# Performance work log

Hardware: AMD Instinct MI355X
Metric: run time of the kernel (lower is better)

Reference implementation:

```python
import jax, jax.numpy as jnp
import numpy as np

COST_CLASS, COST_BBOX, COST_GIOU = 2.0, 5.0, 2.0
ALPHA, GAMMA = 0.25, 2.0
EPS = 1e-8
N_CANDIDATE = 10


def box_cxcywh_to_xyxy(b):
    cx, cy, w, h = b[..., 0], b[..., 1], b[..., 2], b[..., 3]
    return jnp.stack([cx - 0.5 * w, cy - 0.5 * h, cx + 0.5 * w, cy + 0.5 * h], axis=-1)


def pairwise_iou_giou(b1, b2):
    # b1: [N,4] xyxy, b2: [M,4] xyxy -> iou [N,M], giou [N,M]
    area1 = (b1[:, 2] - b1[:, 0]) * (b1[:, 3] - b1[:, 1])
    area2 = (b2[:, 2] - b2[:, 0]) * (b2[:, 3] - b2[:, 1])
    lt = jnp.maximum(b1[:, None, :2], b2[None, :, :2])
    rb = jnp.minimum(b1[:, None, 2:], b2[None, :, 2:])
    wh = jnp.clip(rb - lt, 0.0)
    inter = wh[..., 0] * wh[..., 1]
    union = area1[:, None] + area2[None, :] - inter
    iou = inter / (union + EPS)
    # smallest enclosing box
    lt_c = jnp.minimum(b1[:, None, :2], b2[None, :, :2])
    rb_c = jnp.maximum(b1[:, None, 2:], b2[None, :, 2:])
    wh_c = jnp.clip(rb_c - lt_c, 0.0)
    area_c = wh_c[..., 0] * wh_c[..., 1]
    giou = iou - (area_c - union) / (area_c + EPS)
    return iou, giou


def _match_one(logits, boxes, labels, tboxes):
    # logits [Q,C], boxes [Q,4] cxcywh, labels [G] int, tboxes [G,4] cxcywh
    Q = logits.shape[0]
    G = labels.shape[0]
    prob = jax.nn.sigmoid(logits)                 # [Q,C]  (use_focal_loss path)
    p = prob[:, labels]                           # [Q,G] gather at GT classes
    neg_cost = (1.0 - ALPHA) * p ** GAMMA * (-jnp.log1p(-p + EPS))
    pos_cost = ALPHA * (1.0 - p) ** GAMMA * (-jnp.log(p + EPS))
    cost_class = pos_cost - neg_cost              # [Q,G]
    cost_bbox = jnp.sum(jnp.abs(boxes[:, None, :] - tboxes[None, :, :]), axis=-1)  # L1 cdist [Q,G]
    iou, giou = pairwise_iou_giou(box_cxcywh_to_xyxy(boxes), box_cxcywh_to_xyxy(tboxes))
    C = COST_BBOX * cost_bbox + COST_CLASS * cost_class + COST_GIOU * (-giou)      # [Q,G]

    # --- SimOTA matching (simota_matching), vectorized over GT ---
    cost = C.T                                    # [G,Q]
    ious = iou.T                                  # [G,Q]
    n_cand = min(N_CANDIDATE, Q)
    topk_ious, _ = jax.lax.top_k(ious, n_cand)    # [G,n_cand]
    dynamic_ks = jnp.clip(jnp.sum(topk_ious, axis=1).astype(jnp.int32), 1)  # [G]
    # rank of each anchor per GT under ascending cost
    ranks = jnp.argsort(jnp.argsort(cost, axis=1), axis=1)                  # [G,Q]
    matching = (ranks < dynamic_ks[:, None]).astype(cost.dtype)             # [G,Q]
    # resolve anchors matched to multiple GTs: keep argmin-cost GT
    anchor_matching_gt = matching.sum(axis=0)     # [Q]
    cost_argmin = jnp.argmin(cost, axis=0)        # [Q]
    onehot_min = (jnp.arange(G)[:, None] == cost_argmin[None, :]).astype(cost.dtype)
    matching = jnp.where(anchor_matching_gt[None, :] > 1, onehot_min, matching)
    return jnp.stack([cost, matching], axis=0)    # [2,G,Q]


def reference(pred_logits, pred_boxes, tgt_labels, tgt_boxes):
    # per-image cost blocks + SimOTA matching matrices: [bs, 2, G, Q]
    return jax.vmap(_match_one)(pred_logits, pred_boxes, tgt_labels, tgt_boxes)


def setup_inputs() -> dict:
    key = jax.random.key(0)
    k1, k2, k3, k4 = jax.random.split(key, 4)
    bs, Q, C, G = 16, 4000, 80, 128
    pred_logits = jax.random.normal(k1, (bs, Q, C), dtype=jnp.float32)
    pred_boxes = jax.random.uniform(k2, (bs, Q, 4), dtype=jnp.float32, minval=0.05, maxval=0.95)
    tgt_labels = jax.random.randint(k3, (bs, G), 0, C)
    tgt_boxes = jax.random.uniform(k4, (bs, G, 4), dtype=jnp.float32, minval=0.05, maxval=0.95)
    return {"pred_logits": pred_logits, "pred_boxes": pred_boxes,
            "tgt_labels": tgt_labels, "tgt_boxes": tgt_boxes}
```

## Files before the change

kernel.cpp:

```cpp
#include <hip/hip_runtime.h>
#include <cmath>
#include <cfloat>
#include <climits>


static constexpr int BS = 16;
static constexpr int Qn = 4000;
static constexpr int Cn = 80;
static constexpr int Gn = 128;
static constexpr float kEPS = 1e-8f;


static constexpr size_t kThrvOff = 0;
static constexpr size_t kThriOff = 8 * 1024;
static constexpr size_t kFOff    = 16 * 1024;
static constexpr size_t kFBytes  = (size_t)BS * Cn * Qn * sizeof(float);

__device__ __forceinline__ float focal_cost(float l) {
    const float p = 1.0f / (1.0f + expf(-l));
    const float neg = (0.75f * (p * p)) * (-log1pf(-p + kEPS));
    const float pos = (0.25f * ((1.0f - p) * (1.0f - p))) * (-logf(p + kEPS));
    return pos - neg;
}

__global__ __launch_bounds__(256) void kP_focal(
    const float* __restrict__ logits,
    float* __restrict__ F)
{
    const int b  = blockIdx.y;
    const int q0 = blockIdx.x * 32;
    const int t  = threadIdx.x;

    __shared__ float s_f[32 * 81];

    const float* src = logits + ((size_t)b * Qn + q0) * Cn;
#pragma unroll
    for (int i = 0; i < 10; ++i) {
        const int idx = t + i * 256;
        const int ql = idx / 80, c = idx % 80;
        s_f[ql * 81 + c] = focal_cost(src[idx]);
    }
    __syncthreads();

    float* dst = F + (size_t)b * Cn * Qn;
#pragma unroll
    for (int i = 0; i < 10; ++i) {
        const int j = t + i * 256;
        const int c = j >> 5, ql = j & 31;
        dst[(size_t)c * Qn + q0 + ql] = s_f[ql * 81 + c];
    }
}

__device__ __forceinline__ unsigned long long pack_ci(float c, int q) {
    const unsigned int u = __float_as_uint(c + 0.0f);
    const unsigned int s = (u & 0x80000000u) ? ~u : (u | 0x80000000u);
    return ((unsigned long long)s << 32) | (unsigned int)q;
}

__device__ __forceinline__ unsigned long long shfl_xor_u64(unsigned long long v, int m) {
    const int lo = __shfl_xor((int)(unsigned int)v, m, 64);
    const int hi = __shfl_xor((int)(unsigned int)(v >> 32), m, 64);
    return ((unsigned long long)(unsigned int)hi << 32) | (unsigned int)lo;
}

__device__ __forceinline__ unsigned long long bitonic64_asc_u64(unsigned long long v, int lane) {
#pragma unroll
    for (int k = 2; k <= 64; k <<= 1) {
#pragma unroll
        for (int j = 32; j >= 1; j >>= 1) {
            if (j < k) {
                const unsigned long long o = shfl_xor_u64(v, j);
                const bool up = ((lane & k) == 0);
                const bool keepmin = (((lane & j) == 0) == up);
                const bool omin = (o < v);
                v = (keepmin == omin) ? o : v;
            }
        }
    }
    return v;
}

__device__ __forceinline__ float bitonic64_asc_f32(float v, int lane) {
#pragma unroll
    for (int k = 2; k <= 64; k <<= 1) {
#pragma unroll
        for (int j = 32; j >= 1; j >>= 1) {
            if (j < k) {
                const float o = __shfl_xor(v, j, 64);
                const bool up = ((lane & k) == 0);
                const bool keepmin = (((lane & j) == 0) == up);
                const bool omin = (o < v);
                v = (keepmin == omin) ? o : v;
            }
        }
    }
    return v;
}

__device__ __forceinline__ void ins10_vi(float (&cv)[10], int (&ci)[10],
                                         float v, int q) {
    bool le[10];
#pragma unroll
    for (int j = 0; j < 10; ++j) le[j] = (cv[j] <= v);
#pragma unroll
    for (int j = 9; j >= 1; --j) {
        const float nv = le[j] ? cv[j] : (le[j - 1] ? v : cv[j - 1]);
        const int   ni = le[j] ? ci[j] : (le[j - 1] ? q : ci[j - 1]);
        cv[j] = nv; ci[j] = ni;
    }
    if (!le[0]) { cv[0] = v; ci[0] = q; }
}

__device__ __forceinline__ void ins10_desc(float (&iv)[10], float v) {
    bool ge[10];
#pragma unroll
    for (int j = 0; j < 10; ++j) ge[j] = (iv[j] >= v);
#pragma unroll
    for (int j = 9; j >= 1; --j)
        iv[j] = ge[j] ? iv[j] : (ge[j - 1] ? v : iv[j - 1]);
    if (!ge[0]) iv[0] = v;
}

template <bool USE_F>
__global__ __launch_bounds__(512, 8) void kF(
    const float* __restrict__ boxes,
    const int*   __restrict__ labels,
    const float* __restrict__ tboxes,
    const float* __restrict__ logits,
    const float* __restrict__ F,
    float* __restrict__ out,
    float* __restrict__ thrv,
    int*   __restrict__ thri)
{
    const int lane = threadIdx.x & 63;
    const int w8   = threadIdx.x >> 6;
    const int sub  = w8 & 3;
    const int r    = blockIdx.x;
    const int b    = r >> 7;
    const int g    = r & (Gn - 1);

    const float* tb = tboxes + (size_t)r * 4;
    const float tcx = tb[0], tcy = tb[1], tw = tb[2], th = tb[3];
    const float tx0 = tcx - 0.5f * tw, ty0 = tcy - 0.5f * th;
    const float tx1 = tcx + 0.5f * tw, ty1 = tcy + 0.5f * th;
    const float tarea = (tx1 - tx0) * (ty1 - ty0);

    const float4* brow = reinterpret_cast<const float4*>(boxes) + (size_t)b * Qn;

    __shared__ float              s_st[8][1024];
    __shared__ unsigned long long s_ccb[4][64];
    __shared__ float              s_icb[4][64];
    __shared__ int                s_cnt[8];
    __shared__ unsigned long long s_ce[4][12];
    __shared__ float              s_if[4][12];

    if (lane == 0) s_cnt[w8] = 0;

    if (w8 < 4) {
        const int lab = labels[r];
        const float* Frow = USE_F ? (F + ((size_t)b * Cn + lab) * Qn) : nullptr;
        const float* lcol = USE_F ? nullptr : (logits + (size_t)b * Qn * Cn + lab);
        float* crow = out + (size_t)(b * 2) * Gn * Qn + (size_t)g * Qn;

        float m0 = INFINITY, m1 = INFINITY;

#pragma unroll
        for (int it = 0; it < 4; ++it) {
            const int q0 = it * 1024 + sub * 256 + (lane << 2);
            if ((it < 3) || (q0 < Qn)) {
                float cls4[4];
                if (USE_F) {
                    const float4 f4 = *reinterpret_cast<const float4*>(Frow + q0);
                    cls4[0] = f4.x; cls4[1] = f4.y; cls4[2] = f4.z; cls4[3] = f4.w;
                } else {
#pragma unroll
                    for (int e = 0; e < 4; ++e)
                        cls4[e] = focal_cost(lcol[(size_t)(q0 + e) * Cn]);
                }
                float c4[4];
#pragma unroll
                for (int e = 0; e < 4; ++e) {
                    const float cls = cls4[e];
                    const float4 bb = brow[q0 + e];
                    const float cx = bb.x, cy = bb.y, w = bb.z, h = bb.w;
                    const float x0 = cx - 0.5f * w, y0 = cy - 0.5f * h;
                    const float x1 = cx + 0.5f * w, y1 = cy + 0.5f * h;
                    const float area1 = (x1 - x0) * (y1 - y0);
                    const float l1 = ((fabsf(cx - tcx) + fabsf(cy - tcy))
                                      + fabsf(w - tw)) + fabsf(h - th);
                    const float ltx = fmaxf(x0, tx0), lty = fmaxf(y0, ty0);
                    const float rbx = fminf(x1, tx1), rby = fminf(y1, ty1);
                    const float iw = fmaxf(rbx - ltx, 0.0f), ih = fmaxf(rby - lty, 0.0f);
                    const float inter = iw * ih;
                    const float uni = (area1 + tarea) - inter;
                    const float iou = inter / (uni + kEPS);
                    const float cltx = fminf(x0, tx0), clty = fminf(y0, ty0);
                    const float crbx = fmaxf(x1, tx1), crby = fmaxf(y1, ty1);
                    const float cw = fmaxf(crbx - cltx, 0.0f), ch = fmaxf(crby - clty, 0.0f);
                    const float areac = cw * ch;
                    const float giou = iou - (areac - uni) / (areac + kEPS);

                    const float cost = (5.0f * l1 + 2.0f * cls) + 2.0f * (-giou);
                    c4[e] = cost;
                    const bool le0 = (m0 <= cost), le1 = (m1 <= cost);
                    m1 = le1 ? m1 : (le0 ? cost : m0);
                    m0 = le0 ? m0 : cost;
                }
                float4 cv4; cv4.x = c4[0]; cv4.y = c4[1]; cv4.z = c4[2]; cv4.w = c4[3];
                *reinterpret_cast<float4*>(crow + q0) = cv4;
                *reinterpret_cast<float4*>(&s_st[w8][it * 256 + (lane << 2)]) = cv4;
            }
        }

        float T = 0.0f;
#pragma unroll
        for (int t = 0; t < 10; ++t) {
            float m = m0;
#pragma unroll
            for (int d = 1; d <= 32; d <<= 1)
                m = fminf(m, __shfl_xor(m, d, 64));
            T = m;
            const bool own0 = (m0 == m);
            const unsigned long long bal = __ballot(own0);
            if (own0 && lane == __ffsll((long long)bal) - 1) { m0 = m1; m1 = INFINITY; }
        }

#pragma unroll
        for (int it = 0; it < 4; ++it) {
            const int q0 = it * 1024 + sub * 256 + (lane << 2);
            if ((it < 3) || (q0 < Qn)) {
                const float4 c4 = *reinterpret_cast<const float4*>(
                    &s_st[w8][it * 256 + (lane << 2)]);
#pragma unroll
                for (int e = 0; e < 4; ++e) {
                    const float c = (e == 0) ? c4.x : (e == 1) ? c4.y
                                  : (e == 2) ? c4.z : c4.w;
                    if (c <= T) {
                        const int slot = atomicAdd(&s_cnt[w8], 1);
                        if (slot < 64) s_ccb[sub][slot] = pack_ci(c, q0 + e);
                    }
                }
            }
        }

        const int cnt = s_cnt[w8];
        if (cnt <= 64) {
            unsigned long long v = (lane < cnt) ? s_ccb[sub][lane] : ~0ull;
            v = bitonic64_asc_u64(v, lane);
            if (lane < 12) s_ce[sub][lane] = (lane < 10) ? v : ~0ull;
        } else {
            float cv[10]; int ci[10];
#pragma unroll
            for (int j = 0; j < 10; ++j) { cv[j] = INFINITY; ci[j] = INT_MAX; }
#pragma unroll
            for (int it = 0; it < 4; ++it) {
                const int q0 = it * 1024 + sub * 256 + (lane << 2);
                if ((it < 3) || (q0 < Qn)) {
                    const float4 c4 = *reinterpret_cast<const float4*>(
                        &s_st[w8][it * 256 + (lane << 2)]);
                    ins10_vi(cv, ci, c4.x, q0);
                    ins10_vi(cv, ci, c4.y, q0 + 1);
                    ins10_vi(cv, ci, c4.z, q0 + 2);
                    ins10_vi(cv, ci, c4.w, q0 + 3);
                }
            }
#pragma unroll
            for (int t = 0; t < 10; ++t) {
                float m = cv[0];
#pragma unroll
                for (int d = 1; d <= 32; d <<= 1)
                    m = fminf(m, __shfl_xor(m, d, 64));
                int cq = (cv[0] == m) ? ci[0] : INT_MAX;
#pragma unroll
                for (int d = 1; d <= 32; d <<= 1)
                    cq = min(cq, __shfl_xor(cq, d, 64));
                if (lane == 0) s_ce[sub][t] = pack_ci(m, cq);
                const bool own = (cv[0] == m) && (ci[0] == cq);
                if (own) {
#pragma unroll
                    for (int j = 0; j < 9; ++j) { cv[j] = cv[j + 1]; ci[j] = ci[j + 1]; }
                    cv[9] = INFINITY; ci[9] = INT_MAX;
                }
            }
            if (lane < 2) s_ce[sub][10 + lane] = ~0ull;
        }
    } else {
        float M0 = -INFINITY, M1 = -INFINITY;

#pragma unroll
        for (int it = 0; it < 4; ++it) {
            const int q0 = it * 1024 + sub * 256 + (lane << 2);
            if ((it < 3) || (q0 < Qn)) {
                float io4[4];
#pragma unroll
                for (int e = 0; e < 4; ++e) {
                    const float4 bb = brow[q0 + e];
                    const float x0 = bb.x - 0.5f * bb.z, y0 = bb.y - 0.5f * bb.w;
                    const float x1 = bb.x + 0.5f * bb.z, y1 = bb.y + 0.5f * bb.w;
                    const float area1 = (x1 - x0) * (y1 - y0);
                    const float ltx = fmaxf(x0, tx0), lty = fmaxf(y0, ty0);
                    const float rbx = fminf(x1, tx1), rby = fminf(y1, ty1);
                    const float iw = fmaxf(rbx - ltx, 0.0f), ih = fmaxf(rby - lty, 0.0f);
                    const float inter = iw * ih;
                    const float uni = (area1 + tarea) - inter;
                    const float iou = inter / (uni + kEPS);
                    io4[e] = iou;
                    const bool ge0 = (M0 >= iou), ge1 = (M1 >= iou);
                    M1 = ge1 ? M1 : (ge0 ? iou : M0);
                    M0 = ge0 ? M0 : iou;
                }
                float4 iv4; iv4.x = io4[0]; iv4.y = io4[1]; iv4.z = io4[2]; iv4.w = io4[3];
                *reinterpret_cast<float4*>(&s_st[w8][it * 256 + (lane << 2)]) = iv4;
            }
        }

        float T = 0.0f;
#pragma unroll
        for (int t = 0; t < 10; ++t) {
            float m = M0;
#pragma unroll
            for (int d = 1; d <= 32; d <<= 1)
                m = fmaxf(m, __shfl_xor(m, d, 64));
            T = m;
            const bool own0 = (M0 == m);
            const unsigned long long bal = __ballot(own0);
            if (own0 && lane == __ffsll((long long)bal) - 1) { M0 = M1; M1 = -INFINITY; }
        }

#pragma unroll
        for (int it = 0; it < 4; ++it) {
            const int q0 = it * 1024 + sub * 256 + (lane << 2);
            if ((it < 3) || (q0 < Qn)) {
                const float4 c4 = *reinterpret_cast<const float4*>(
                    &s_st[w8][it * 256 + (lane << 2)]);
#pragma unroll
                for (int e = 0; e < 4; ++e) {
                    const float c = (e == 0) ? c4.x : (e == 1) ? c4.y
                                  : (e == 2) ? c4.z : c4.w;
                    if (c >= T) {
                        const int slot = atomicAdd(&s_cnt[w8], 1);
                        if (slot < 64) s_icb[sub][slot] = c;
                    }
                }
            }
        }

        const int cnt = s_cnt[w8];
        if (cnt <= 64) {
            float v = (lane < cnt) ? s_icb[sub][lane] : -INFINITY;
            v = bitonic64_asc_f32(v, lane);
            if (lane >= 54) s_if[sub][63 - lane] = v;
            if (lane < 2) s_if[sub][10 + lane] = -INFINITY;
        } else {
            float iv[10];
#pragma unroll
            for (int j = 0; j < 10; ++j) iv[j] = -INFINITY;
#pragma unroll
            for (int it = 0; it < 4; ++it) {
                const int q0 = it * 1024 + sub * 256 + (lane << 2);
                if ((it < 3) || (q0 < Qn)) {
                    const float4 c4 = *reinterpret_cast<const float4*>(
                        &s_st[w8][it * 256 + (lane << 2)]);
                    ins10_desc(iv, c4.x);
                    ins10_desc(iv, c4.y);
                    ins10_desc(iv, c4.z);
                    ins10_desc(iv, c4.w);
                }
            }
#pragma unroll
            for (int t = 0; t < 10; ++t) {
                float m = iv[0];
#pragma unroll
                for (int d = 1; d <= 32; d <<= 1)
                    m = fmaxf(m, __shfl_xor(m, d, 64));
                if (lane == 0) s_if[sub][t] = m;
                const bool own0 = (iv[0] == m);
                const unsigned long long bal = __ballot(own0);
                if (own0 && lane == __ffsll((long long)bal) - 1) {
#pragma unroll
                    for (int j = 0; j < 9; ++j) iv[j] = iv[j + 1];
                    iv[9] = -INFINITY;
                }
            }
            if (lane < 2) s_if[sub][10 + lane] = -INFINITY;
        }
    }

    __syncthreads();

    if (threadIdx.x == 0) {
        int p0 = 0, p1 = 0, p2 = 0, p3 = 0;
        float s = 0.0f;
#pragma unroll
        for (int t = 0; t < 10; ++t) {
            const float a0 = s_if[0][p0], a1 = s_if[1][p1];
            const float a2 = s_if[2][p2], a3 = s_if[3][p3];
            const float mx = fmaxf(fmaxf(a0, a1), fmaxf(a2, a3));
            if (a0 == mx) ++p0;
            else if (a1 == mx) ++p1;
            else if (a2 == mx) ++p2;
            else ++p3;
            s += mx;
        }
        int k = (int)s;
        if (k < 1) k = 1;
        if (k > 10) k = 10;

        p0 = 0; p1 = 0; p2 = 0; p3 = 0;
        unsigned long long key = 0;
#pragma unroll
        for (int t = 0; t < 10; ++t) {
            const unsigned long long a0 = s_ce[0][p0], a1 = s_ce[1][p1];
            const unsigned long long a2 = s_ce[2][p2], a3 = s_ce[3][p3];
            unsigned long long mn = a0;
            if (a1 < mn) mn = a1;
            if (a2 < mn) mn = a2;
            if (a3 < mn) mn = a3;
            if (a0 == mn) ++p0;
            else if (a1 == mn) ++p1;
            else if (a2 == mn) ++p2;
            else ++p3;
            if (t == k - 1) key = mn;
        }
        const unsigned int su = (unsigned int)(key >> 32);
        thrv[r] = __uint_as_float((su & 0x80000000u) ? (su ^ 0x80000000u) : ~su);
        thri[r] = (int)(unsigned int)key;
    }
}

__global__ __launch_bounds__(512) void kC4(
    const float* __restrict__ outc,
    const float* __restrict__ thrv,
    const int*   __restrict__ thri,
    float* __restrict__ out)
{
    const int b  = blockIdx.y;
    const int lq = threadIdx.x & 63;
    const int gh = threadIdx.x >> 6;
    const int q  = blockIdx.x * 64 + lq;

    __shared__ float          s_tv[Gn];
    __shared__ int            s_ti[Gn];
    __shared__ unsigned short s_mask[8][64];
    __shared__ float          s_mv[8][64];
    __shared__ int            s_mg[8][64];

    if (threadIdx.x < Gn) {
        s_tv[threadIdx.x] = thrv[b * Gn + threadIdx.x];
        s_ti[threadIdx.x] = thri[b * Gn + threadIdx.x];
    }
    __syncthreads();

    const float* crow = outc + (size_t)(b * 2) * Gn * Qn + q;
    unsigned mask = 0;
    float mv = INFINITY;
    int mg = 0;
    const int gbase = gh * 16;
    if (q < Qn) {
#pragma unroll
        for (int j = 0; j < 16; ++j) {
            const int g = gbase + j;
            const float c = crow[(size_t)g * Qn];
            const bool mt = (c < s_tv[g]) || (c == s_tv[g] && q <= s_ti[g]);
            mask |= (unsigned)mt << j;
            if (c < mv) { mv = c; mg = g; }
        }
    }
    s_mask[gh][lq] = (unsigned short)mask;
    s_mv[gh][lq]   = mv;
    s_mg[gh][lq]   = mg;
    __syncthreads();

    int cnt = 0;
#pragma unroll
    for (int h = 0; h < 8; ++h) cnt += __popc((unsigned)s_mask[h][lq]);
    float bmv = s_mv[0][lq];
    int   bmg = s_mg[0][lq];
#pragma unroll
    for (int h = 1; h < 8; ++h) {
        const float v = s_mv[h][lq];
        if (v < bmv) { bmv = v; bmg = s_mg[h][lq]; }
    }
    const bool fix = (cnt > 1);

    if (q < Qn) {
        float* mrow = out + (size_t)(b * 2 + 1) * Gn * Qn + q;
#pragma unroll
        for (int j = 0; j < 16; ++j) {
            const int g = gbase + j;
            const bool bit = (mask >> j) & 1u;
            const bool mt = fix ? (g == bmg) : bit;
            mrow[(size_t)g * Qn] = mt ? 1.0f : 0.0f;
        }
    }
}

extern "C" void kernel_launch(void* const* d_in, const int* in_sizes, int n_in,
                              void* d_out, int out_size, void* d_ws, size_t ws_size,
                              hipStream_t stream) {
    (void)in_sizes; (void)n_in; (void)out_size;
    const float* logits = (const float*)d_in[0];
    const float* boxes  = (const float*)d_in[1];
    const int*   labels = (const int*)d_in[2];
    const float* tboxes = (const float*)d_in[3];
    float* out = (float*)d_out;

    float* thrv = (float*)((char*)d_ws + kThrvOff);
    int*   thri = (int*)  ((char*)d_ws + kThriOff);
    float* F    = (float*)((char*)d_ws + kFOff);

    const bool use_f = (ws_size >= kFOff + kFBytes);

    dim3 gF(BS * Gn);
    if (use_f) {
        dim3 gP(Qn / 32, BS);
        kP_focal<<<gP, 256, 0, stream>>>(logits, F);
        kF<true><<<gF, 512, 0, stream>>>(boxes, labels, tboxes, logits, F,
                                         out, thrv, thri);
    } else {
        kF<false><<<gF, 512, 0, stream>>>(boxes, labels, tboxes, logits, nullptr,
                                          out, thrv, thri);
    }

    dim3 gC((Qn + 63) / 64, BS);
    kC4<<<gC, 512, 0, stream>>>(out, thrv, thri, out);
}
```

Baseline: 77.61 us.

## Fuse cost and IoU selection per wave, split Q across eight waves

Previously four waves computed the cost rows and top-10 cost while four other waves recomputed IoU separately. Now all eight waves each handle a 512-wide slice of Q, computing cost and IoU in a single pass, so the box geometry is computed once. Candidate compaction uses ballot/popcount prefix sums in place of shared-memory atomics. The final thread-0 merge now combines eight sorted lists instead of four, which makes that serial step longer.

After: 89.36 us. 15.1% more time.

```diff
diff --git a/kernel.cpp b/kernel.cpp
--- a/kernel.cpp
+++ b/kernel.cpp
@@ -134,7 +134,6 @@
 {
     const int lane = threadIdx.x & 63;
     const int w8   = threadIdx.x >> 6;
-    const int sub  = w8 & 3;
     const int r    = blockIdx.x;
     const int b    = r >> 7;
     const int g    = r & (Gn - 1);
@@ -146,280 +145,258 @@
     const float tarea = (tx1 - tx0) * (ty1 - ty0);
 
     const float4* brow = reinterpret_cast<const float4*>(boxes) + (size_t)b * Qn;
-
-    __shared__ float              s_st[8][1024];
-    __shared__ unsigned long long s_ccb[4][64];
-    __shared__ float              s_icb[4][64];
-    __shared__ int                s_cnt[8];
-    __shared__ unsigned long long s_ce[4][12];
-    __shared__ float              s_if[4][12];
-
-    if (lane == 0) s_cnt[w8] = 0;
-
-    if (w8 < 4) {
-        const int lab = labels[r];
-        const float* Frow = USE_F ? (F + ((size_t)b * Cn + lab) * Qn) : nullptr;
-        const float* lcol = USE_F ? nullptr : (logits + (size_t)b * Qn * Cn + lab);
-        float* crow = out + (size_t)(b * 2) * Gn * Qn + (size_t)g * Qn;
-
-        float m0 = INFINITY, m1 = INFINITY;
-
-#pragma unroll
-        for (int it = 0; it < 4; ++it) {
-            const int q0 = it * 1024 + sub * 256 + (lane << 2);
-            if ((it < 3) || (q0 < Qn)) {
-                float cls4[4];
-                if (USE_F) {
-                    const float4 f4 = *reinterpret_cast<const float4*>(Frow + q0);
-                    cls4[0] = f4.x; cls4[1] = f4.y; cls4[2] = f4.z; cls4[3] = f4.w;
-                } else {
-#pragma unroll
-                    for (int e = 0; e < 4; ++e)
-                        cls4[e] = focal_cost(lcol[(size_t)(q0 + e) * Cn]);
-                }
-                float c4[4];
-#pragma unroll
-                for (int e = 0; e < 4; ++e) {
-                    const float cls = cls4[e];
-                    const float4 bb = brow[q0 + e];
-                    const float cx = bb.x, cy = bb.y, w = bb.z, h = bb.w;
-                    const float x0 = cx - 0.5f * w, y0 = cy - 0.5f * h;
-                    const float x1 = cx + 0.5f * w, y1 = cy + 0.5f * h;
-                    const float area1 = (x1 - x0) * (y1 - y0);
-                    const float l1 = ((fabsf(cx - tcx) + fabsf(cy - tcy))
-                                      + fabsf(w - tw)) + fabsf(h - th);
-                    const float ltx = fmaxf(x0, tx0), lty = fmaxf(y0, ty0);
-                    const float rbx = fminf(x1, tx1), rby = fminf(y1, ty1);
-                    const float iw = fmaxf(rbx - ltx, 0.0f), ih = fmaxf(rby - lty, 0.0f);
-                    const float inter = iw * ih;
-                    const float uni = (area1 + tarea) - inter;
-                    const float iou = inter / (uni + kEPS);
-                    const float cltx = fminf(x0, tx0), clty = fminf(y0, ty0);
-                    const float crbx = fmaxf(x1, tx1), crby = fmaxf(y1, ty1);
-                    const float cw = fmaxf(crbx - cltx, 0.0f), ch = fmaxf(crby - clty, 0.0f);
-                    const float areac = cw * ch;
-                    const float giou = iou - (areac - uni) / (areac + kEPS);
-
-                    const float cost = (5.0f * l1 + 2.0f * cls) + 2.0f * (-giou);
-                    c4[e] = cost;
-                    const bool le0 = (m0 <= cost), le1 = (m1 <= cost);
-                    m1 = le1 ? m1 : (le0 ? cost : m0);
-                    m0 = le0 ? m0 : cost;
-                }
-                float4 cv4; cv4.x = c4[0]; cv4.y = c4[1]; cv4.z = c4[2]; cv4.w = c4[3];
-                *reinterpret_cast<float4*>(crow + q0) = cv4;
-                *reinterpret_cast<float4*>(&s_st[w8][it * 256 + (lane << 2)]) = cv4;
-            }
-        }
-
-        float T = 0.0f;
+    const int lab = labels[r];
+    const float* Frow = USE_F ? (F + ((size_t)b * Cn + lab) * Qn) : nullptr;
+    const float* lcol = USE_F ? nullptr : (logits + (size_t)b * Qn * Cn + lab);
+    float* crow = out + (size_t)(b * 2) * Gn * Qn + (size_t)g * Qn;
+
+    __shared__ float              s_cost[8][512];
+    __shared__ float              s_iou[8][512];
+    __shared__ unsigned long long s_ccb[8][64];
+    __shared__ float              s_icb[8][64];
+    __shared__ unsigned long long s_ce[8][10];
+    __shared__ float              s_if[8][10];
+
+    float m0 = INFINITY, m1 = INFINITY;
+    float M0 = -INFINITY, M1 = -INFINITY;
+
+#pragma unroll
+    for (int it = 0; it < 2; ++it) {
+        const int q0 = it * 2048 + w8 * 256 + (lane << 2);
+        if ((it < 1) || (q0 < Qn)) {
+            float cls4[4];
+            if (USE_F) {
+                const float4 f4 = *reinterpret_cast<const float4*>(Frow + q0);
+                cls4[0] = f4.x; cls4[1] = f4.y; cls4[2] = f4.z; cls4[3] = f4.w;
+            } else {
+#pragma unroll
+                for (int e = 0; e < 4; ++e)
+                    cls4[e] = focal_cost(lcol[(size_t)(q0 + e) * Cn]);
+            }
+            float c4[4], io4[4];
+#pragma unroll
+            for (int e = 0; e < 4; ++e) {
+                const float cls = cls4[e];
+                const float4 bb = brow[q0 + e];
+                const float cx = bb.x, cy = bb.y, w = bb.z, h = bb.w;
+                const float x0 = cx - 0.5f * w, y0 = cy - 0.5f * h;
+                const float x1 = cx + 0.5f * w, y1 = cy + 0.5f * h;
+                const float area1 = (x1 - x0) * (y1 - y0);
+                const float l1 = ((fabsf(cx - tcx) + fabsf(cy - tcy))
+                                  + fabsf(w - tw)) + fabsf(h - th);
+                const float ltx = fmaxf(x0, tx0), lty = fmaxf(y0, ty0);
+                const float rbx = fminf(x1, tx1), rby = fminf(y1, ty1);
+                const float iw = fmaxf(rbx - ltx, 0.0f), ih = fmaxf(rby - lty, 0.0f);
+                const float inter = iw * ih;
+                const float uni = (area1 + tarea) - inter;
+                const float iou = inter / (uni + kEPS);
+                const float cltx = fminf(x0, tx0), clty = fminf(y0, ty0);
+                const float crbx = fmaxf(x1, tx1), crby = fmaxf(y1, ty1);
+                const float cw = fmaxf(crbx - cltx, 0.0f), ch = fmaxf(crby - clty, 0.0f);
+                const float areac = cw * ch;
+                const float giou = iou - (areac - uni) / (areac + kEPS);
+
+                const float cost = (5.0f * l1 + 2.0f * cls) + 2.0f * (-giou);
+                c4[e] = cost; io4[e] = iou;
+                const bool le0 = (m0 <= cost), le1 = (m1 <= cost);
+                m1 = le1 ? m1 : (le0 ? cost : m0);
+                m0 = le0 ? m0 : cost;
+                const bool ge0 = (M0 >= iou), ge1 = (M1 >= iou);
+                M1 = ge1 ? M1 : (ge0 ? iou : M0);
+                M0 = ge0 ? M0 : iou;
+            }
+            float4 cv4; cv4.x = c4[0]; cv4.y = c4[1]; cv4.z = c4[2]; cv4.w = c4[3];
+            float4 iv4; iv4.x = io4[0]; iv4.y = io4[1]; iv4.z = io4[2]; iv4.w = io4[3];
+            *reinterpret_cast<float4*>(crow + q0) = cv4;
+            *reinterpret_cast<float4*>(&s_cost[w8][it * 256 + (lane << 2)]) = cv4;
+            *reinterpret_cast<float4*>(&s_iou[w8][it * 256 + (lane << 2)]) = iv4;
+        }
+    }
+
+    float Tc = 0.0f;
+#pragma unroll
+    for (int t = 0; t < 10; ++t) {
+        float m = m0;
+#pragma unroll
+        for (int d = 1; d <= 32; d <<= 1)
+            m = fminf(m, __shfl_xor(m, d, 64));
+        Tc = m;
+        const bool own0 = (m0 == m);
+        const unsigned long long bal = __ballot(own0);
+        if (own0 && lane == __ffsll((long long)bal) - 1) { m0 = m1; m1 = INFINITY; }
+    }
+    float Ti = 0.0f;
+#pragma unroll
+    for (int t = 0; t < 10; ++t) {
+        float m = M0;
+#pragma unroll
+        for (int d = 1; d <= 32; d <<= 1)
+            m = fmaxf(m, __shfl_xor(m, d, 64));
+        Ti = m;
+        const bool own0 = (M0 == m);
+        const unsigned long long bal = __ballot(own0);
+        if (own0 && lane == __ffsll((long long)bal) - 1) { M0 = M1; M1 = -INFINITY; }
+    }
+
+    const unsigned long long lmask = (1ull << lane) - 1ull;
+    int basec = 0, basei = 0;
+#pragma unroll
+    for (int it = 0; it < 2; ++it) {
+        const int q0 = it * 2048 + w8 * 256 + (lane << 2);
+        const bool inb = (it < 1) || (q0 < Qn);
+        const int st = it * 256 + (lane << 2);
+        const float4 c4 = *reinterpret_cast<const float4*>(&s_cost[w8][st]);
+        const float4 i4 = *reinterpret_cast<const float4*>(&s_iou[w8][st]);
+#pragma unroll
+        for (int e = 0; e < 4; ++e) {
+            const float c = (e == 0) ? c4.x : (e == 1) ? c4.y : (e == 2) ? c4.z : c4.w;
+            const bool pc = inb && (c <= Tc);
+            const unsigned long long balc = __ballot(pc);
+            if (pc) {
+                const int slot = basec + __popcll(balc & lmask);
+                if (slot < 64) s_ccb[w8][slot] = pack_ci(c, q0 + e);
+            }
+            basec += __popcll(balc);
+
+            const float v = (e == 0) ? i4.x : (e == 1) ? i4.y : (e == 2) ? i4.z : i4.w;
+            const bool pi = inb && (v >= Ti);
+            const unsigned long long bali = __ballot(pi);
+            if (pi) {
+                const int slot = basei + __popcll(bali & lmask);
+                if (slot < 64) s_icb[w8][slot] = v;
+            }
+            basei += __popcll(bali);
+        }
+    }
+
+    if (basec <= 64) {
+        unsigned long long v = (lane < basec) ? s_ccb[w8][lane] : ~0ull;
+        v = bitonic64_asc_u64(v, lane);
+        if (lane < 10) s_ce[w8][lane] = v;
+    } else {
+        float cv[10]; int ci[10];
+#pragma unroll
+        for (int j = 0; j < 10; ++j) { cv[j] = INFINITY; ci[j] = INT_MAX; }
+#pragma unroll
+        for (int it = 0; it < 2; ++it) {
+            const int q0 = it * 2048 + w8 * 256 + (lane << 2);
+            if ((it < 1) || (q0 < Qn)) {
+                const float4 c4 = *reinterpret_cast<const float4*>(
+                    &s_cost[w8][it * 256 + (lane << 2)]);
+                ins10_vi(cv, ci, c4.x, q0);
+                ins10_vi(cv, ci, c4.y, q0 + 1);
+                ins10_vi(cv, ci, c4.z, q0 + 2);
+                ins10_vi(cv, ci, c4.w, q0 + 3);
+            }
+        }
 #pragma unroll
         for (int t = 0; t < 10; ++t) {
-            float m = m0;
+            float m = cv[0];
 #pragma unroll
             for (int d = 1; d <= 32; d <<= 1)
                 m = fminf(m, __shfl_xor(m, d, 64));
-            T = m;
-            const bool own0 = (m0 == m);
-            const unsigned long long bal = __ballot(own0);
-            if (own0 && lane == __ffsll((long long)bal) - 1) { m0 = m1; m1 = INFINITY; }
-        }
-
-#pragma unroll
-        for (int it = 0; it < 4; ++it) {
-            const int q0 = it * 1024 + sub * 256 + (lane << 2);
-            if ((it < 3) || (q0 < Qn)) {
-                const float4 c4 = *reinterpret_cast<const float4*>(
-                    &s_st[w8][it * 256 + (lane << 2)]);
-#pragma unroll
-                for (int e = 0; e < 4; ++e) {
-                    const float c = (e == 0) ? c4.x : (e == 1) ? c4.y
-                                  : (e == 2) ? c4.z : c4.w;
-                    if (c <= T) {
-                        const int slot = atomicAdd(&s_cnt[w8], 1);
-                        if (slot < 64) s_ccb[sub][slot] = pack_ci(c, q0 + e);
-                    }
-                }
-            }
-        }
-
-        const int cnt = s_cnt[w8];
-        if (cnt <= 64) {
-            unsigned long long v = (lane < cnt) ? s_ccb[sub][lane] : ~0ull;
-            v = bitonic64_asc_u64(v, lane);
-            if (lane < 12) s_ce[sub][lane] = (lane < 10) ? v : ~0ull;
-        } else {
-            float cv[10]; int ci[10];
-#pragma unroll
-            for (int j = 0; j < 10; ++j) { cv[j] = INFINITY; ci[j] = INT_MAX; }
-#pragma unroll
-            for (int it = 0; it < 4; ++it) {
-                const int q0 = it * 1024 + sub * 256 + (lane << 2);
-                if ((it < 3) || (q0 < Qn)) {
-                    const float4 c4 = *reinterpret_cast<const float4*>(
-                        &s_st[w8][it * 256 + (lane << 2)]);
-                    ins10_vi(cv, ci, c4.x, q0);
-                    ins10_vi(cv, ci, c4.y, q0 + 1);
-                    ins10_vi(cv, ci, c4.z, q0 + 2);
-                    ins10_vi(cv, ci, c4.w, q0 + 3);
-                }
-            }
-#pragma unroll
-            for (int t = 0; t < 10; ++t) {
-                float m = cv[0];
-#pragma unroll
-                for (int d = 1; d <= 32; d <<= 1)
-                    m = fminf(m, __shfl_xor(m, d, 64));
-                int cq = (cv[0] == m) ? ci[0] : INT_MAX;
-#pragma unroll
-                for (int d = 1; d <= 32; d <<= 1)
-                    cq = min(cq, __shfl_xor(cq, d, 64));
-                if (lane == 0) s_ce[sub][t] = pack_ci(m, cq);
-                const bool own = (cv[0] == m) && (ci[0] == cq);
-                if (own) {
-#pragma unroll
-                    for (int j = 0; j < 9; ++j) { cv[j] = cv[j + 1]; ci[j] = ci[j + 1]; }
-                    cv[9] = INFINITY; ci[9] = INT_MAX;
-                }
-            }
-            if (lane < 2) s_ce[sub][10 + lane] = ~0ull;
-        }
+            int cq = (cv[0] == m) ? ci[0] : INT_MAX;
+#pragma unroll
+            for (int d = 1; d <= 32; d <<= 1)
+                cq = min(cq, __shfl_xor(cq, d, 64));
+            if (lane == 0) s_ce[w8][t] = pack_ci(m, cq);
+            const bool own = (cv[0] == m) && (ci[0] == cq);
+            if (own) {
+#pragma unroll
+                for (int j = 0; j < 9; ++j) { cv[j] = cv[j + 1]; ci[j] = ci[j + 1]; }
+                cv[9] = INFINITY; ci[9] = INT_MAX;
+            }
+        }
+    }
+
+    if (basei <= 64) {
+        float v = (lane < basei) ? s_icb[w8][lane] : -INFINITY;
+        v = bitonic64_asc_f32(v, lane);
+        if (lane >= 54) s_if[w8][63 - lane] = v;
     } else {
-        float M0 = -INFINITY, M1 = -INFINITY;
-
-#pragma unroll
-        for (int it = 0; it < 4; ++it) {
-            const int q0 = it * 1024 + sub * 256 + (lane << 2);
-            if ((it < 3) || (q0 < Qn)) {
-                float io4[4];
-#pragma unroll
-                for (int e = 0; e < 4; ++e) {
-                    const float4 bb = brow[q0 + e];
-                    const float x0 = bb.x - 0.5f * bb.z, y0 = bb.y - 0.5f * bb.w;
-                    const float x1 = bb.x + 0.5f * bb.z, y1 = bb.y + 0.5f * bb.w;
-                    const float area1 = (x1 - x0) * (y1 - y0);
-                    const float ltx = fmaxf(x0, tx0), lty = fmaxf(y0, ty0);
-                    const float rbx = fminf(x1, tx1), rby = fminf(y1, ty1);
-                    const float iw = fmaxf(rbx - ltx, 0.0f), ih = fmaxf(rby - lty, 0.0f);
-                    const float inter = iw * ih;
-                    const float uni = (area1 + tarea) - inter;
-                    const float iou = inter / (uni + kEPS);
-                    io4[e] = iou;
-                    const bool ge0 = (M0 >= iou), ge1 = (M1 >= iou);
-                    M1 = ge1 ? M1 : (ge0 ? iou : M0);
-                    M0 = ge0 ? M0 : iou;
-                }
-                float4 iv4; iv4.x = io4[0]; iv4.y = io4[1]; iv4.z = io4[2]; iv4.w = io4[3];
-                *reinterpret_cast<float4*>(&s_st[w8][it * 256 + (lane << 2)]) = iv4;
-            }
-        }
-
-        float T = 0.0f;
+        float iv[10];
+#pragma unroll
+        for (int j = 0; j < 10; ++j) iv[j] = -INFINITY;
+#pragma unroll
+        for (int it = 0; it < 2; ++it) {
+            const int q0 = it * 2048 + w8 * 256 + (lane << 2);
+            if ((it < 1) || (q0 < Qn)) {
+                const float4 i4 = *reinterpret_cast<const float4*>(
+                    &s_iou[w8][it * 256 + (lane << 2)]);
+                ins10_desc(iv, i4.x);
+                ins10_desc(iv, i4.y);
+                ins10_desc(iv, i4.z);
+                ins10_desc(iv, i4.w);
+            }
+        }
 #pragma unroll
         for (int t = 0; t < 10; ++t) {
-            float m = M0;
+            float m = iv[0];
 #pragma unroll
             for (int d = 1; d <= 32; d <<= 1)
                 m = fmaxf(m, __shfl_xor(m, d, 64));
-            T = m;
-            const bool own0 = (M0 == m);
+            if (lane == 0) s_if[w8][t] = m;
+            const bool own0 = (iv[0] == m);
             const unsigned long long bal = __ballot(own0);
-            if (own0 && lane == __ffsll((long long)bal) - 1) { M0 = M1; M1 = -INFINITY; }
-        }
-
-#pragma unroll
-        for (int it = 0; it < 4; ++it) {
-            const int q0 = it * 1024 + sub * 256 + (lane << 2);
-            if ((it < 3) || (q0 < Qn)) {
-                const float4 c4 = *reinterpret_cast<const float4*>(
-                    &s_st[w8][it * 256 + (lane << 2)]);
-#pragma unroll
-                for (int e = 0; e < 4; ++e) {
-                    const float c = (e == 0) ? c4.x : (e == 1) ? c4.y
-                                  : (e == 2) ? c4.z : c4.w;
-                    if (c >= T) {
-                        const int slot = atomicAdd(&s_cnt[w8], 1);
-                        if (slot < 64) s_icb[sub][slot] = c;
-                    }
-                }
-            }
-        }
-
-        const int cnt = s_cnt[w8];
-        if (cnt <= 64) {
-            float v = (lane < cnt) ? s_icb[sub][lane] : -INFINITY;
-            v = bitonic64_asc_f32(v, lane);
-            if (lane >= 54) s_if[sub][63 - lane] = v;
-            if (lane < 2) s_if[sub][10 + lane] = -INFINITY;
-        } else {
-            float iv[10];
-#pragma unroll
-            for (int j = 0; j < 10; ++j) iv[j] = -INFINITY;
-#pragma unroll
-            for (int it = 0; it < 4; ++it) {
-                const int q0 = it * 1024 + sub * 256 + (lane << 2);
-                if ((it < 3) || (q0 < Qn)) {
-                    const float4 c4 = *reinterpret_cast<const float4*>(
-                        &s_st[w8][it * 256 + (lane << 2)]);
-                    ins10_desc(iv, c4.x);
-                    ins10_desc(iv, c4.y);
-                    ins10_desc(iv, c4.z);
-                    ins10_desc(iv, c4.w);
-                }
-            }
-#pragma unroll
-            for (int t = 0; t < 10; ++t) {
-                float m = iv[0];
-#pragma unroll
-                for (int d = 1; d <= 32; d <<= 1)
-                    m = fmaxf(m, __shfl_xor(m, d, 64));
-                if (lane == 0) s_if[sub][t] = m;
-                const bool own0 = (iv[0] == m);
-                const unsigned long long bal = __ballot(own0);
-                if (own0 && lane == __ffsll((long long)bal) - 1) {
-#pragma unroll
-                    for (int j = 0; j < 9; ++j) iv[j] = iv[j + 1];
-                    iv[9] = -INFINITY;
-                }
-            }
-            if (lane < 2) s_if[sub][10 + lane] = -INFINITY;
+            if (own0 && lane == __ffsll((long long)bal) - 1) {
+#pragma unroll
+                for (int j = 0; j < 9; ++j) iv[j] = iv[j + 1];
+                iv[9] = -INFINITY;
+            }
         }
     }
 
     __syncthreads();
 
     if (threadIdx.x == 0) {
-        int p0 = 0, p1 = 0, p2 = 0, p3 = 0;
+        int p0 = 0, p1 = 0, p2 = 0, p3 = 0, p4 = 0, p5 = 0, p6 = 0, p7 = 0;
         float s = 0.0f;
 #pragma unroll
         for (int t = 0; t < 10; ++t) {
             const float a0 = s_if[0][p0], a1 = s_if[1][p1];
             const float a2 = s_if[2][p2], a3 = s_if[3][p3];
-            const float mx = fmaxf(fmaxf(a0, a1), fmaxf(a2, a3));
-            if (a0 == mx) ++p0;
+            const float a4 = s_if[4][p4], a5 = s_if[5][p5];
+            const float a6 = s_if[6][p6], a7 = s_if[7][p7];
+            const float mx = fmaxf(fmaxf(fmaxf(a0, a1), fmaxf(a2, a3)),
+                                   fmaxf(fmaxf(a4, a5), fmaxf(a6, a7)));
+            if      (a0 == mx) ++p0;
             else if (a1 == mx) ++p1;
             else if (a2 == mx) ++p2;
-            else ++p3;
+            else if (a3 == mx) ++p3;
+            else if (a4 == mx) ++p4;
+            else if (a5 == mx) ++p5;
+            else if (a6 == mx) ++p6;
+            else               ++p7;
             s += mx;
         }
         int k = (int)s;
         if (k < 1) k = 1;
         if (k > 10) k = 10;
 
-        p0 = 0; p1 = 0; p2 = 0; p3 = 0;
+        p0 = 0; p1 = 0; p2 = 0; p3 = 0; p4 = 0; p5 = 0; p6 = 0; p7 = 0;
         unsigned long long key = 0;
 #pragma unroll
         for (int t = 0; t < 10; ++t) {
             const unsigned long long a0 = s_ce[0][p0], a1 = s_ce[1][p1];
             const unsigned long long a2 = s_ce[2][p2], a3 = s_ce[3][p3];
+            const unsigned long long a4 = s_ce[4][p4], a5 = s_ce[5][p5];
+            const unsigned long long a6 = s_ce[6][p6], a7 = s_ce[7][p7];
             unsigned long long mn = a0;
             if (a1 < mn) mn = a1;
             if (a2 < mn) mn = a2;
             if (a3 < mn) mn = a3;
-            if (a0 == mn) ++p0;
+            if (a4 < mn) mn = a4;
+            if (a5 < mn) mn = a5;
+            if (a6 < mn) mn = a6;
+            if (a7 < mn) mn = a7;
+            if      (a0 == mn) ++p0;
             else if (a1 == mn) ++p1;
             else if (a2 == mn) ++p2;
-            else ++p3;
+            else if (a3 == mn) ++p3;
+            else if (a4 == mn) ++p4;
+            else if (a5 == mn) ++p5;
+            else if (a6 == mn) ++p6;
+            else               ++p7;
             if (t == k - 1) key = mn;
         }
         const unsigned int su = (unsigned int)(key >> 32);
```
